# Performance work log

Hardware: AMD Instinct MI355X
Metric: run time of the kernel (lower is better)

The kernel has to match this reference:

```python
import jax, jax.numpy as jnp
import numpy as np

NUM_HEADS = 32
NUM_KV_HEADS = 8
HEAD_DIM = 128
ROPE_THETA = 10000.0


def _rope_cos_sin(seq_len, head_dim, dtype):
    # [seq, head_dim/2] angles, duplicated to [seq, head_dim] via concat (rotate-half convention)
    inv_freq = 1.0 / (ROPE_THETA ** (jnp.arange(0, head_dim, 2, dtype=jnp.float32) / head_dim))
    ang = jnp.arange(seq_len, dtype=jnp.float32)[:, None] * inv_freq[None, :]
    ang = jnp.concatenate([ang, ang], axis=-1)
    return jnp.cos(ang).astype(dtype), jnp.sin(ang).astype(dtype)


def _rotate_half(x):
    d = x.shape[-1] // 2
    return jnp.concatenate([-x[..., d:], x[..., :d]], axis=-1)


def setup_inputs() -> dict:
    key = jax.random.key(0)
    ks = jax.random.split(key, 5)
    E = NUM_HEADS * HEAD_DIM
    KVE = NUM_KV_HEADS * HEAD_DIM
    B, S = 2, 2048
    sc_in = 1.0 / np.sqrt(E)
    return {
        "x": jax.random.normal(ks[0], (B, S, E), jnp.float32),
        "Wq": jax.random.normal(ks[1], (E, E), jnp.float32) * sc_in,
        "Wk": jax.random.normal(ks[2], (E, KVE), jnp.float32) * sc_in,
        "Wv": jax.random.normal(ks[3], (E, KVE), jnp.float32) * sc_in,
        "Wo": jax.random.normal(ks[4], (E, E), jnp.float32) * sc_in,
    }


def reference(x, Wq, Wk, Wv, Wo):
    b, s, e = x.shape
    H, KV, D = NUM_HEADS, NUM_KV_HEADS, HEAD_DIM
    G = H // KV
    scale = 1.0 / np.sqrt(D)

    q = (x @ Wq).reshape(b, s, H, D).transpose(0, 2, 1, 3)    # [b,H,s,D]
    k = (x @ Wk).reshape(b, s, KV, D).transpose(0, 2, 1, 3)   # [b,KV,s,D]
    v = (x @ Wv).reshape(b, s, KV, D).transpose(0, 2, 1, 3)   # [b,KV,s,D]

    cos, sin = _rope_cos_sin(s, D, q.dtype)                   # [s,D]
    q = q * cos + _rotate_half(q) * sin
    k = k * cos + _rotate_half(k) * sin

    # GQA: group q heads by kv head instead of repeat_interleaving k/v
    qg = q.reshape(b, KV, G, s, D)
    attn = jnp.einsum("bkgqd,bkvd->bkgqv", qg, k) * scale     # [b,KV,G,s,s]

    causal = jnp.where(
        jnp.arange(s)[:, None] >= jnp.arange(s)[None, :], 0.0, -jnp.inf
    ).astype(jnp.float32)
    attn = attn.astype(jnp.float32) + causal
    attn = jax.nn.softmax(attn, axis=-1).astype(q.dtype)

    out = jnp.einsum("bkgqv,bkvd->bkgqd", attn, v)            # [b,KV,G,s,D]
    out = out.reshape(b, H, s, D).transpose(0, 2, 1, 3).reshape(b, s, H * D)
    return out @ Wo
```

## Files before the change

### kernel.cpp

```cpp
#include <hip/hip_runtime.h>
#include <stdint.h>
#include <math.h>

typedef short bf16x8 __attribute__((ext_vector_type(8)));
typedef float f32x4 __attribute__((ext_vector_type(4)));

#if __has_builtin(__builtin_amdgcn_exp2f)
#define EXP2F(x) __builtin_amdgcn_exp2f(x)
#else
#define EXP2F(x) exp2f(x)
#endif

static constexpr int Bn   = 2;
static constexpr int Sn   = 2048;
static constexpr int NH   = 32;
static constexpr int NKV  = 8;
static constexpr int Dh   = 128;
static constexpr int En   = NH * Dh;
static constexpr int KVEn = NKV * Dh;
static constexpr int QKVE = En + 2 * KVEn;
static constexpr int MT   = Bn * Sn;
static constexpr int QT   = Sn / 128;

__device__ __forceinline__ unsigned short f2bf(float f) {
  unsigned int u = __float_as_uint(f);
  u += 0x7FFFu + ((u >> 16) & 1u);
  return (unsigned short)(u >> 16);
}
__device__ __forceinline__ float bf2f(unsigned short h) {
  return __uint_as_float(((unsigned int)h) << 16);
}

typedef __attribute__((address_space(1))) void* gas_t;
typedef __attribute__((address_space(3))) void* las_t;
__device__ __forceinline__ void gl_lds16(const void* g, void* l) {
  __builtin_amdgcn_global_load_lds((gas_t)(uintptr_t)g, (las_t)(uint32_t)(uintptr_t)l,
                                   16, 0, 0);
}

#define VMW(n)  asm volatile("s_waitcnt vmcnt(" #n ")" ::: "memory")
#define LGKM0   asm volatile("s_waitcnt lgkmcnt(0)" ::: "memory")
#define SCHEDB  __builtin_amdgcn_sched_barrier(0)
#define BAR     __builtin_amdgcn_s_barrier()


__global__ void cast_bf16_kernel(const float* __restrict__ x,
                                 unsigned short* __restrict__ y, int n4) {
  int i = blockIdx.x * 256 + threadIdx.x;
  if (i >= n4) return;
  float4 v = ((const float4*)x)[i];
  ushort4 o;
  o.x = f2bf(v.x); o.y = f2bf(v.y); o.z = f2bf(v.z); o.w = f2bf(v.w);
  ((ushort4*)y)[i] = o;
}

__global__ void tcast_kernel(const float* __restrict__ W,
                             unsigned short* __restrict__ WT, int R, int C) {
  __shared__ float t[32][33];
  int tx = threadIdx.x, ty = threadIdx.y;
  int c = blockIdx.x * 32 + tx, r = blockIdx.y * 32 + ty;
  t[ty][tx] = W[(size_t)r * C + c];
  __syncthreads();
  int ro = blockIdx.x * 32 + ty, co = blockIdx.y * 32 + tx;
  WT[(size_t)ro * R + co] = f2bf(t[tx][ty]);
}

__global__ void rope_table_kernel(float2* __restrict__ cs) {
  int i = blockIdx.x * 256 + threadIdx.x;
  int s = i >> 6, d = i & 63;
  float inv = powf(10000.0f, -(float)d * (1.0f / 64.0f));
  float a = (float)s * inv;
  cs[i] = make_float2(cosf(a), sinf(a));
}

__global__ void rope_kernel(unsigned short* __restrict__ q,
                            const float2* __restrict__ cs, int rowstride, float scl) {
  int row = blockIdx.x;
  int s = row & (Sn - 1);
  int hl = threadIdx.x >> 6, d = threadIdx.x & 63;
  int h = blockIdx.y * 4 + hl;
  size_t base = (size_t)row * rowstride + (size_t)h * Dh + d;
  float2 c = cs[s * 64 + d];
  float x0 = bf2f(q[base]), x1 = bf2f(q[base + 64]);
  q[base]      = f2bf((x0 * c.x - x1 * c.y) * scl);
  q[base + 64] = f2bf((x1 * c.x + x0 * c.y) * scl);
}

__global__ void vtrans_kernel(const unsigned short* __restrict__ V, int rowstride,
                              unsigned short* __restrict__ Vt) {
  __shared__ unsigned short t[32][33];
  int bk = blockIdx.z;
  int b = bk >> 3, kv = bk & 7;
  int d = blockIdx.x * 32 + threadIdx.x;
  int s = blockIdx.y * 32 + threadIdx.y;
  t[threadIdx.y][threadIdx.x] = V[(size_t)(b * Sn + s) * rowstride + kv * Dh + d];
  __syncthreads();
  int dd = blockIdx.x * 32 + threadIdx.y;
  int so = blockIdx.y * 32 + threadIdx.x;
  Vt[((size_t)bk * Dh + dd) * Sn + so] = t[threadIdx.x][threadIdx.y];
}


__global__ __launch_bounds__(512, 2) void gemm256_kernel(
    const unsigned short* __restrict__ A, const unsigned short* __restrict__ BT,
    void* __restrict__ Cout, int M, int N, int K, int out_f32) {
  __shared__ unsigned short lds[2][4][128 * 64];
  const int tid = threadIdx.x;
  const int lane = tid & 63, wave = tid >> 6;
  const int r15 = lane & 15, kg = lane >> 4;
  const int wr = wave >> 2, wc = wave & 3;
  const int m0 = blockIdx.y * 256, n0 = blockIdx.x * 256;
  const char* Ab = (const char*)A;
  const char* Bb = (const char*)BT;
  const int KT = K >> 6;

  f32x4 acc[2][2][4][2] = {};
  bf16x8 ar[4][2];
  bf16x8 br[2][2][2];

#define STAGE_H(SRC, ROW0, KT_, SLOT)                                         \
  do {                                                                        \
    _Pragma("unroll") for (int ld = 0; ld < 2; ++ld) {                        \
      int _f = (ld * 512 + tid) * 16;                                         \
      int _row = _f >> 7, _cb = _f & 127;                                     \
      gl_lds16(SRC + ((size_t)((ROW0) + _row) * K + (KT_) * 64) * 2 +         \
                   (_cb ^ ((_row & 7) << 4)),                                 \
               (char*)(SLOT) + _f);                                           \
    }                                                                         \
  } while (0)

#define GPHASE(MH, NH, BUF, DO_LDA, DO_LDB, STAGE_STMT, WAIT_STMT)            \
  do {                                                                        \
    if (DO_LDA) {                                                             \
      const char* _as = (const char*)lds[BUF][MH];                            \
      _Pragma("unroll") for (int mf = 0; mf < 4; ++mf) {                      \
        int _r = wr * 64 + mf * 16 + r15;                                     \
        int _sw = (_r & 7) << 4;                                              \
        ar[mf][0] = *(const bf16x8*)(_as + _r * 128 + ((kg * 16) ^ _sw));     \
        ar[mf][1] = *(const bf16x8*)(_as + _r * 128 + ((64 + kg * 16) ^ _sw));\
      }                                                                       \
    }                                                                         \
    if (DO_LDB) {                                                             \
      const char* _bs = (const char*)lds[BUF][2 + NH];                        \
      _Pragma("unroll") for (int nf = 0; nf < 2; ++nf) {                      \
        int _r = wc * 32 + nf * 16 + r15;                                     \
        int _sw = (_r & 7) << 4;                                              \
        br[NH][nf][0] =                                                       \
            *(const bf16x8*)(_bs + _r * 128 + ((kg * 16) ^ _sw));             \
        br[NH][nf][1] =                                                       \
            *(const bf16x8*)(_bs + _r * 128 + ((64 + kg * 16) ^ _sw));        \
      }                                                                       \
    }                                                                         \
    STAGE_STMT;                                                               \
    BAR;                                                                      \
    if ((DO_LDA) || (DO_LDB)) { LGKM0; }                                      \
    SCHEDB;                                                                   \
    __builtin_amdgcn_s_setprio(1);                                            \
    _Pragma("unroll") for (int mf = 0; mf < 4; ++mf)                          \
      _Pragma("unroll") for (int nf = 0; nf < 2; ++nf) {                      \
        acc[MH][NH][mf][nf] = __builtin_amdgcn_mfma_f32_16x16x32_bf16(        \
            ar[mf][0], br[NH][nf][0], acc[MH][NH][mf][nf], 0, 0, 0);          \
        acc[MH][NH][mf][nf] = __builtin_amdgcn_mfma_f32_16x16x32_bf16(        \
            ar[mf][1], br[NH][nf][1], acc[MH][NH][mf][nf], 0, 0, 0);          \
      }                                                                       \
    __builtin_amdgcn_s_setprio(0);                                            \
    SCHEDB;                                                                   \
    WAIT_STMT;                                                                \
    BAR;                                                                      \
    SCHEDB;                                                                   \
  } while (0)

  STAGE_H(Ab, m0,       0, lds[0][0]);
  STAGE_H(Bb, n0,       0, lds[0][2]);
  STAGE_H(Ab, m0 + 128, 0, lds[0][1]);
  STAGE_H(Bb, n0 + 128, 0, lds[0][3]);
  STAGE_H(Ab, m0,       1, lds[1][0]);
  STAGE_H(Bb, n0,       1, lds[1][2]);
  VMW(8);
  SCHEDB;
  BAR;
  SCHEDB;

  for (int k = 0; k + 2 < KT; k += 2) {
    GPHASE(0, 0, 0, true,  true,  STAGE_H(Ab, m0 + 128, k + 1, lds[1][1]), VMW(6));
    GPHASE(0, 1, 0, false, true,  STAGE_H(Bb, n0 + 128, k + 1, lds[1][3]), VMW(10));
    GPHASE(1, 0, 0, true,  false, STAGE_H(Ab, m0,       k + 2, lds[0][0]), (void)0);
    GPHASE(1, 1, 0, false, false, STAGE_H(Bb, n0,       k + 2, lds[0][2]), VMW(8));
    GPHASE(0, 0, 1, true,  true,  STAGE_H(Ab, m0 + 128, k + 2, lds[0][1]), VMW(6));
    GPHASE(0, 1, 1, false, true,  STAGE_H(Bb, n0 + 128, k + 2, lds[0][3]), VMW(10));
    GPHASE(1, 0, 1, true,  false, STAGE_H(Ab, m0,       k + 3, lds[1][0]), (void)0);
    GPHASE(1, 1, 1, false, false, STAGE_H(Bb, n0,       k + 3, lds[1][2]), VMW(8));
  }
  GPHASE(0, 0, 0, true,  true,  STAGE_H(Ab, m0 + 128, KT - 1, lds[1][1]), VMW(6));
  GPHASE(0, 1, 0, false, true,  STAGE_H(Bb, n0 + 128, KT - 1, lds[1][3]), VMW(10));
  GPHASE(1, 0, 0, true,  false, (void)0, (void)0);
  GPHASE(1, 1, 0, false, false, (void)0, VMW(0));
  GPHASE(0, 0, 1, true,  true,  (void)0, (void)0);
  GPHASE(0, 1, 1, false, true,  (void)0, (void)0);
  GPHASE(1, 0, 1, true,  false, (void)0, (void)0);
  GPHASE(1, 1, 1, false, false, (void)0, (void)0);

#undef GPHASE
#undef STAGE_H

#pragma unroll
  for (int mh = 0; mh < 2; ++mh)
#pragma unroll
    for (int nh = 0; nh < 2; ++nh)
#pragma unroll
      for (int mf = 0; mf < 4; ++mf)
#pragma unroll
        for (int nf = 0; nf < 2; ++nf)
#pragma unroll
          for (int t = 0; t < 4; ++t) {
            int row = m0 + mh * 128 + wr * 64 + mf * 16 + kg * 4 + t;
            int col = n0 + nh * 128 + wc * 32 + nf * 16 + r15;
            if (out_f32)
              ((float*)Cout)[(size_t)row * N + col] = acc[mh][nh][mf][nf][t];
            else
              ((unsigned short*)Cout)[(size_t)row * N + col] =
                  f2bf(acc[mh][nh][mf][nf][t]);
          }
}


__device__ __forceinline__ void sm_update(f32x4 sc[4], f32x4 o[8],
                                          float mrow[4], float lrow[4],
                                          bool diag, int qrow0, int kt,
                                          int r15, int kg, char* Pw) {
  if (diag) {
#pragma unroll
    for (int kf = 0; kf < 4; ++kf) {
      int kvg = kt * 64 + kf * 16 + r15;
#pragma unroll
      for (int t = 0; t < 4; ++t)
        if (kvg > qrow0 + kg * 4 + t) sc[kf][t] = -1e30f;
    }
  }
  float mx[4], sm[4];
#pragma unroll
  for (int t = 0; t < 4; ++t) {
    float v = fmaxf(fmaxf(sc[0][t], sc[1][t]), fmaxf(sc[2][t], sc[3][t]));
#pragma unroll
    for (int off = 1; off < 16; off <<= 1) v = fmaxf(v, __shfl_xor(v, off, 16));
    mx[t] = fmaxf(mrow[t], v);
    sm[t] = EXP2F(mrow[t] - mx[t]);
    mrow[t] = mx[t];
  }
#pragma unroll
  for (int kf = 0; kf < 4; ++kf)
#pragma unroll
    for (int t = 0; t < 4; ++t) sc[kf][t] = EXP2F(sc[kf][t] - mx[t]);
#pragma unroll
  for (int t = 0; t < 4; ++t) {
    float v = sc[0][t] + sc[1][t] + sc[2][t] + sc[3][t];
#pragma unroll
    for (int off = 1; off < 16; off <<= 1) v += __shfl_xor(v, off, 16);
    lrow[t] = lrow[t] * sm[t] + v;
  }
#pragma unroll
  for (int nf = 0; nf < 8; ++nf)
#pragma unroll
    for (int t = 0; t < 4; ++t) o[nf][t] *= sm[t];
#pragma unroll
  for (int kf = 0; kf < 4; ++kf)
#pragma unroll
    for (int t = 0; t < 4; ++t) {
      int r = kg * 4 + t, c = kf * 16 + r15;
      *(unsigned short*)(Pw + r * 128 + ((c * 2) ^ ((r & 7) << 4))) = f2bf(sc[kf][t]);
    }
}

__global__ __launch_bounds__(512, 4) void attn_kernel(
    const unsigned short* __restrict__ Q, const unsigned short* __restrict__ Kl,
    const unsigned short* __restrict__ Vt, unsigned short* __restrict__ AO) {
  __shared__ unsigned short Ks[2][64 * 128];
  __shared__ unsigned short Vs[2][128 * 64];
  __shared__ unsigned short Ps[8][16 * 64];
  const int tid = threadIdx.x, lane = tid & 63, wave = tid >> 6;
  const int h = blockIdx.x, b = blockIdx.z;
  const int qt = (QT - 1) - blockIdx.y;
  const int kvh = h >> 2;
  const int r15 = lane & 15, kg = lane >> 4;
  const int qrow0 = qt * 128 + wave * 16;
  const int kmax = 2 * qt + 2;

  bf16x8 qf[4];
#pragma unroll
  for (int db = 0; db < 4; ++db)
    qf[db] = *(const bf16x8*)&Q[(size_t)(b * Sn + qrow0 + r15) * QKVE +
                                h * Dh + db * 32 + kg * 8];

  f32x4 o[8] = {};
  float mrow[4] = {-1e30f, -1e30f, -1e30f, -1e30f};
  float lrow[4] = {0.f, 0.f, 0.f, 0.f};

  const char* Kbase = (const char*)Kl + (size_t)(b * Sn) * (QKVE * 2) + kvh * 256;
  const char* Vbase = (const char*)Vt + (size_t)((b * NKV + kvh) * Dh) * (Sn * 2);

  auto stage = [&](int kt, int bi) {
#pragma unroll
    for (int c = 0; c < 2; ++c) {
      int f = (c * 512 + tid) * 16;
      int row = f >> 8, cb = f & 255;
      gl_lds16(Kbase + (size_t)(kt * 64 + row) * (QKVE * 2) + (cb ^ ((row & 7) << 4)),
               (char*)Ks[bi] + f);
    }
#pragma unroll
    for (int c = 0; c < 2; ++c) {
      int f = (c * 512 + tid) * 16;
      int row = f >> 7, cb = f & 127;
      gl_lds16(Vbase + (size_t)row * (Sn * 2) + kt * 128 + (cb ^ ((row & 7) << 4)),
               (char*)Vs[bi] + f);
    }
  };

  stage(0, 0);
  __syncthreads();

  for (int kt = 0; kt < kmax; ++kt) {
    const int cur = kt & 1;
    if (kt + 1 < kmax) stage(kt + 1, cur ^ 1);
    if (kt * 64 <= qrow0 + 15) {
      const char* Kc = (const char*)Ks[cur];
      const char* Vc = (const char*)Vs[cur];
      f32x4 sc[4] = {};
      __builtin_amdgcn_s_setprio(1);
#pragma unroll
      for (int db = 0; db < 4; ++db) {
#pragma unroll
        for (int kf = 0; kf < 4; ++kf) {
          int krow = kf * 16 + r15;
          int cb = (db * 32 + kg * 8) * 2;
          bf16x8 kb = *(const bf16x8*)(Kc + krow * 256 + (cb ^ ((krow & 7) << 4)));
          sc[kf] = __builtin_amdgcn_mfma_f32_16x16x32_bf16(qf[db], kb, sc[kf], 0, 0, 0);
        }
      }
      __builtin_amdgcn_s_setprio(0);

      char* Pw = (char*)Ps[wave];
      bool diag = (kt * 64 + 63) > qrow0;
      sm_update(sc, o, mrow, lrow, diag, qrow0, kt, r15, kg, Pw);

      __builtin_amdgcn_s_setprio(1);
#pragma unroll
      for (int ks = 0; ks < 2; ++ks) {
        bf16x8 pa = *(const bf16x8*)(Pw + r15 * 128 + ((kg * 16 + ks * 64) ^ ((r15 & 7) << 4)));
#pragma unroll
        for (int nf = 0; nf < 8; ++nf) {
          int vrow = nf * 16 + r15;
          int cb = (ks * 32 + kg * 8) * 2;
          bf16x8 vb = *(const bf16x8*)(Vc + vrow * 128 + (cb ^ ((vrow & 7) << 4)));
          o[nf] = __builtin_amdgcn_mfma_f32_16x16x32_bf16(pa, vb, o[nf], 0, 0, 0);
        }
      }
      __builtin_amdgcn_s_setprio(0);
    }
    __syncthreads();
  }

  float rinv[4];
#pragma unroll
  for (int t = 0; t < 4; ++t) rinv[t] = 1.0f / lrow[t];
#pragma unroll
  for (int nf = 0; nf < 8; ++nf)
#pragma unroll
    for (int t = 0; t < 4; ++t) {
      int srow = qrow0 + kg * 4 + t;
      AO[(size_t)(b * Sn + srow) * En + h * Dh + nf * 16 + r15] = f2bf(o[nf][t] * rinv[t]);
    }
}


extern "C" void kernel_launch(void* const* d_in, const int* in_sizes, int n_in,
                              void* d_out, int out_size, void* d_ws, size_t ws_size,
                              hipStream_t stream) {
  const float* x  = (const float*)d_in[0];
  const float* Wq = (const float*)d_in[1];
  const float* Wk = (const float*)d_in[2];
  const float* Wv = (const float*)d_in[3];
  const float* Wo = (const float*)d_in[4];

  char* ws = (char*)d_ws;
  size_t off = 0;
  auto alloc = [&](size_t bytes) -> char* {
    char* p = ws + off;
    off += (bytes + 255) & ~(size_t)255;
    return p;
  };
  unsigned short* xb   = (unsigned short*)alloc((size_t)MT * En * 2);
  unsigned short* Wqkv = (unsigned short*)alloc((size_t)QKVE * En * 2);
  unsigned short* WoT  = (unsigned short*)alloc((size_t)En * En * 2);
  unsigned short* Cqkv = (unsigned short*)alloc((size_t)MT * QKVE * 2);
  unsigned short* Vt   = (unsigned short*)alloc((size_t)MT * KVEn * 2);
  float2* cs           = (float2*)alloc((size_t)Sn * 64 * sizeof(float2));
  unsigned short* AO   = xb;

  cast_bf16_kernel<<<MT * (En / 4) / 256, 256, 0, stream>>>(x, xb, MT * En / 4);
  tcast_kernel<<<dim3(En / 32, En / 32), dim3(32, 32), 0, stream>>>(Wq, Wqkv, En, En);
  tcast_kernel<<<dim3(KVEn / 32, En / 32), dim3(32, 32), 0, stream>>>(
      Wk, Wqkv + (size_t)En * En, En, KVEn);
  tcast_kernel<<<dim3(KVEn / 32, En / 32), dim3(32, 32), 0, stream>>>(
      Wv, Wqkv + (size_t)(En + KVEn) * En, En, KVEn);
  tcast_kernel<<<dim3(En / 32, En / 32), dim3(32, 32), 0, stream>>>(Wo, WoT, En, En);
  rope_table_kernel<<<Sn * 64 / 256, 256, 0, stream>>>(cs);

  gemm256_kernel<<<dim3(QKVE / 256, MT / 256), 512, 0, stream>>>(
      xb, Wqkv, Cqkv, MT, QKVE, En, 0);

  const float scl = 0.08838834764831845f * 1.4426950408889634f;
  rope_kernel<<<dim3(MT, NH / 4), 256, 0, stream>>>(Cqkv, cs, QKVE, scl);
  rope_kernel<<<dim3(MT, NKV / 4), 256, 0, stream>>>(Cqkv + En, cs, QKVE, 1.0f);
  vtrans_kernel<<<dim3(Dh / 32, Sn / 32, Bn * NKV), dim3(32, 32), 0, stream>>>(
      Cqkv + En + KVEn, QKVE, Vt);

  attn_kernel<<<dim3(NH, QT, Bn), 512, 0, stream>>>(Cqkv, Cqkv + En, Vt, AO);

  gemm256_kernel<<<dim3(En / 256, MT / 256), 512, 0, stream>>>(
      AO, WoT, d_out, MT, En, En, 1);
}
```

Before: 617.9 us.

## Restructure GEMM wave tiling to 128x64 per wave with register double-buffered fragments

```diff
diff --git a/kernel.cpp b/kernel.cpp
--- a/kernel.cpp
+++ b/kernel.cpp
@@ -108,119 +108,126 @@
   const int tid = threadIdx.x;
   const int lane = tid & 63, wave = tid >> 6;
   const int r15 = lane & 15, kg = lane >> 4;
-  const int wr = wave >> 2, wc = wave & 3;
+  const int wm = wave >> 2, wn = wave & 3;
+  const int brow0 = (wn & 1) * 64;
   const int m0 = blockIdx.y * 256, n0 = blockIdx.x * 256;
   const char* Ab = (const char*)A;
   const char* Bb = (const char*)BT;
   const int KT = K >> 6;
 
-  f32x4 acc[2][2][4][2] = {};
-  bf16x8 ar[4][2];
-  bf16x8 br[2][2][2];
-
-#define STAGE_H(SRC, ROW0, KT_, SLOT)                                         \
+  f32x4 acc[8][4] = {};
+  bf16x8 a0[4][2], a1[4][2];
+  bf16x8 bb0[4][2], bb1[4][2];
+
+#define STG(SRC, ROW0, TILE, SLOT)                                            \
   do {                                                                        \
     _Pragma("unroll") for (int ld = 0; ld < 2; ++ld) {                        \
       int _f = (ld * 512 + tid) * 16;                                         \
       int _row = _f >> 7, _cb = _f & 127;                                     \
-      gl_lds16(SRC + ((size_t)((ROW0) + _row) * K + (KT_) * 64) * 2 +         \
+      gl_lds16(SRC + ((size_t)((ROW0) + _row) * K + (size_t)(TILE) * 64) * 2 +\
                    (_cb ^ ((_row & 7) << 4)),                                 \
                (char*)(SLOT) + _f);                                           \
     }                                                                         \
   } while (0)
 
-#define GPHASE(MH, NH, BUF, DO_LDA, DO_LDB, STAGE_STMT, WAIT_STMT)            \
+#define RD_A(DST, BUF, MQ)                                                    \
   do {                                                                        \
-    if (DO_LDA) {                                                             \
-      const char* _as = (const char*)lds[BUF][MH];                            \
-      _Pragma("unroll") for (int mf = 0; mf < 4; ++mf) {                      \
-        int _r = wr * 64 + mf * 16 + r15;                                     \
-        int _sw = (_r & 7) << 4;                                              \
-        ar[mf][0] = *(const bf16x8*)(_as + _r * 128 + ((kg * 16) ^ _sw));     \
-        ar[mf][1] = *(const bf16x8*)(_as + _r * 128 + ((64 + kg * 16) ^ _sw));\
-      }                                                                       \
+    const char* _b = (const char*)lds[BUF][wm];                               \
+    _Pragma("unroll") for (int j = 0; j < 4; ++j) {                           \
+      int _r = (MQ) * 64 + j * 16 + r15;                                      \
+      int _s = (_r & 7) << 4;                                                 \
+      DST[j][0] = *(const bf16x8*)(_b + _r * 128 + ((kg * 16) ^ _s));         \
+      DST[j][1] = *(const bf16x8*)(_b + _r * 128 + ((64 + kg * 16) ^ _s));    \
     }                                                                         \
-    if (DO_LDB) {                                                             \
-      const char* _bs = (const char*)lds[BUF][2 + NH];                        \
-      _Pragma("unroll") for (int nf = 0; nf < 2; ++nf) {                      \
-        int _r = wc * 32 + nf * 16 + r15;                                     \
-        int _sw = (_r & 7) << 4;                                              \
-        br[NH][nf][0] =                                                       \
-            *(const bf16x8*)(_bs + _r * 128 + ((kg * 16) ^ _sw));             \
-        br[NH][nf][1] =                                                       \
-            *(const bf16x8*)(_bs + _r * 128 + ((64 + kg * 16) ^ _sw));        \
-      }                                                                       \
+  } while (0)
+
+#define RD_B(DST, BUF)                                                        \
+  do {                                                                        \
+    const char* _b = (const char*)lds[BUF][2 + (wn >> 1)];                    \
+    _Pragma("unroll") for (int f = 0; f < 4; ++f) {                           \
+      int _r = brow0 + f * 16 + r15;                                          \
+      int _s = (_r & 7) << 4;                                                 \
+      DST[f][0] = *(const bf16x8*)(_b + _r * 128 + ((kg * 16) ^ _s));         \
+      DST[f][1] = *(const bf16x8*)(_b + _r * 128 + ((64 + kg * 16) ^ _s));    \
     }                                                                         \
-    STAGE_STMT;                                                               \
-    BAR;                                                                      \
-    if ((DO_LDA) || (DO_LDB)) { LGKM0; }                                      \
-    SCHEDB;                                                                   \
+  } while (0)
+
+#define PH(MQ, NQ, AB, BB, RD, ST, WT, DOBAR)                                 \
+  do {                                                                        \
+    RD;                                                                       \
+    ST;                                                                       \
     __builtin_amdgcn_s_setprio(1);                                            \
-    _Pragma("unroll") for (int mf = 0; mf < 4; ++mf)                          \
-      _Pragma("unroll") for (int nf = 0; nf < 2; ++nf) {                      \
-        acc[MH][NH][mf][nf] = __builtin_amdgcn_mfma_f32_16x16x32_bf16(        \
-            ar[mf][0], br[NH][nf][0], acc[MH][NH][mf][nf], 0, 0, 0);          \
-        acc[MH][NH][mf][nf] = __builtin_amdgcn_mfma_f32_16x16x32_bf16(        \
-            ar[mf][1], br[NH][nf][1], acc[MH][NH][mf][nf], 0, 0, 0);          \
+    _Pragma("unroll") for (int j = 0; j < 4; ++j)                             \
+      _Pragma("unroll") for (int n2 = 0; n2 < 2; ++n2) {                      \
+        acc[(MQ)*4 + j][(NQ)*2 + n2] =                                        \
+            __builtin_amdgcn_mfma_f32_16x16x32_bf16(                          \
+                AB[j][0], BB[(NQ)*2 + n2][0], acc[(MQ)*4 + j][(NQ)*2 + n2],   \
+                0, 0, 0);                                                     \
+        acc[(MQ)*4 + j][(NQ)*2 + n2] =                                        \
+            __builtin_amdgcn_mfma_f32_16x16x32_bf16(                          \
+                AB[j][1], BB[(NQ)*2 + n2][1], acc[(MQ)*4 + j][(NQ)*2 + n2],   \
+                0, 0, 0);                                                     \
       }                                                                       \
     __builtin_amdgcn_s_setprio(0);                                            \
+    LGKM0;                                                                    \
     SCHEDB;                                                                   \
-    WAIT_STMT;                                                                \
-    BAR;                                                                      \
-    SCHEDB;                                                                   \
+    WT;                                                                       \
+    if (DOBAR) { BAR; SCHEDB; }                                               \
   } while (0)
 
-  STAGE_H(Ab, m0,       0, lds[0][0]);
-  STAGE_H(Bb, n0,       0, lds[0][2]);
-  STAGE_H(Ab, m0 + 128, 0, lds[0][1]);
-  STAGE_H(Bb, n0 + 128, 0, lds[0][3]);
-  STAGE_H(Ab, m0,       1, lds[1][0]);
-  STAGE_H(Bb, n0,       1, lds[1][2]);
-  VMW(8);
+  STG(Bb, n0,       0, lds[0][2]); STG(Bb, n0 + 128, 0, lds[0][3]);
+  STG(Ab, m0,       0, lds[0][0]); STG(Ab, m0 + 128, 0, lds[0][1]);
+  STG(Bb, n0,       1, lds[1][2]); STG(Bb, n0 + 128, 1, lds[1][3]);
+  STG(Ab, m0,       1, lds[1][0]); STG(Ab, m0 + 128, 1, lds[1][1]);
+  VMW(0);
   SCHEDB;
   BAR;
   SCHEDB;
-
-  for (int k = 0; k + 2 < KT; k += 2) {
-    GPHASE(0, 0, 0, true,  true,  STAGE_H(Ab, m0 + 128, k + 1, lds[1][1]), VMW(6));
-    GPHASE(0, 1, 0, false, true,  STAGE_H(Bb, n0 + 128, k + 1, lds[1][3]), VMW(10));
-    GPHASE(1, 0, 0, true,  false, STAGE_H(Ab, m0,       k + 2, lds[0][0]), (void)0);
-    GPHASE(1, 1, 0, false, false, STAGE_H(Bb, n0,       k + 2, lds[0][2]), VMW(8));
-    GPHASE(0, 0, 1, true,  true,  STAGE_H(Ab, m0 + 128, k + 2, lds[0][1]), VMW(6));
-    GPHASE(0, 1, 1, false, true,  STAGE_H(Bb, n0 + 128, k + 2, lds[0][3]), VMW(10));
-    GPHASE(1, 0, 1, true,  false, STAGE_H(Ab, m0,       k + 3, lds[1][0]), (void)0);
-    GPHASE(1, 1, 1, false, false, STAGE_H(Bb, n0,       k + 3, lds[1][2]), VMW(8));
+  RD_B(bb0, 0);
+  RD_A(a0, 0, 0);
+  LGKM0;
+  SCHEDB;
+
+  for (int i = 0; i + 1 < (KT >> 1); ++i) {
+    const int t2 = 2 * i + 2, t3 = 2 * i + 3;
+    PH(0, 0, a0, bb0, RD_A(a1, 0, 1), STG(Bb, n0,       t2, lds[0][2]), VMW(8), 1);
+    PH(0, 1, a0, bb0, (void)0,        STG(Bb, n0 + 128, t2, lds[0][3]), VMW(8), 1);
+    PH(1, 0, a1, bb0, RD_B(bb1, 1),
+       STG(Ab, m0, t2, lds[0][0]); STG(Ab, m0 + 128, t2, lds[0][1]),    VMW(8), 1);
+    PH(1, 1, a1, bb0, RD_A(a0, 1, 0), (void)0,                          VMW(8), 1);
+    PH(0, 0, a0, bb1, RD_A(a1, 1, 1), STG(Bb, n0,       t3, lds[1][2]), VMW(8), 1);
+    PH(0, 1, a0, bb1, (void)0,        STG(Bb, n0 + 128, t3, lds[1][3]), VMW(8), 1);
+    PH(1, 0, a1, bb1, RD_B(bb0, 0),
+       STG(Ab, m0, t3, lds[1][0]); STG(Ab, m0 + 128, t3, lds[1][1]),    VMW(8), 1);
+    PH(1, 1, a1, bb1, RD_A(a0, 0, 0), (void)0,                          VMW(8), 1);
   }
-  GPHASE(0, 0, 0, true,  true,  STAGE_H(Ab, m0 + 128, KT - 1, lds[1][1]), VMW(6));
-  GPHASE(0, 1, 0, false, true,  STAGE_H(Bb, n0 + 128, KT - 1, lds[1][3]), VMW(10));
-  GPHASE(1, 0, 0, true,  false, (void)0, (void)0);
-  GPHASE(1, 1, 0, false, false, (void)0, VMW(0));
-  GPHASE(0, 0, 1, true,  true,  (void)0, (void)0);
-  GPHASE(0, 1, 1, false, true,  (void)0, (void)0);
-  GPHASE(1, 0, 1, true,  false, (void)0, (void)0);
-  GPHASE(1, 1, 1, false, false, (void)0, (void)0);
-
-#undef GPHASE
-#undef STAGE_H
-
-#pragma unroll
-  for (int mh = 0; mh < 2; ++mh)
-#pragma unroll
-    for (int nh = 0; nh < 2; ++nh)
-#pragma unroll
-      for (int mf = 0; mf < 4; ++mf)
-#pragma unroll
-        for (int nf = 0; nf < 2; ++nf)
-#pragma unroll
-          for (int t = 0; t < 4; ++t) {
-            int row = m0 + mh * 128 + wr * 64 + mf * 16 + kg * 4 + t;
-            int col = n0 + nh * 128 + wc * 32 + nf * 16 + r15;
-            if (out_f32)
-              ((float*)Cout)[(size_t)row * N + col] = acc[mh][nh][mf][nf][t];
-            else
-              ((unsigned short*)Cout)[(size_t)row * N + col] =
-                  f2bf(acc[mh][nh][mf][nf][t]);
-          }
+  PH(0, 0, a0, bb0, RD_A(a1, 0, 1), (void)0, VMW(4), 1);
+  PH(0, 1, a0, bb0, (void)0,        (void)0, VMW(0), 1);
+  PH(1, 0, a1, bb0, RD_B(bb1, 1),   (void)0, (void)0, 0);
+  PH(1, 1, a1, bb0, RD_A(a0, 1, 0), (void)0, (void)0, 0);
+  PH(0, 0, a0, bb1, RD_A(a1, 1, 1), (void)0, (void)0, 0);
+  PH(0, 1, a0, bb1, (void)0,        (void)0, (void)0, 0);
+  PH(1, 0, a1, bb1, (void)0,        (void)0, (void)0, 0);
+  PH(1, 1, a1, bb1, (void)0,        (void)0, (void)0, 0);
+
+#undef PH
+#undef RD_B
+#undef RD_A
+#undef STG
+
+#pragma unroll
+  for (int mf = 0; mf < 8; ++mf)
+#pragma unroll
+    for (int nf = 0; nf < 4; ++nf)
+#pragma unroll
+      for (int t = 0; t < 4; ++t) {
+        int row = m0 + wm * 128 + mf * 16 + kg * 4 + t;
+        int col = n0 + wn * 64 + nf * 16 + r15;
+        if (out_f32)
+          ((float*)Cout)[(size_t)row * N + col] = acc[mf][nf][t];
+        else
+          ((unsigned short*)Cout)[(size_t)row * N + col] = f2bf(acc[mf][nf][t]);
+      }
 }
 
 
```

Result: slower. 1.592 ms (+157.6%).

## Software-pipeline LDS fragment reads one phase ahead in GEMM main loop

Applied to the files above, without the earlier changes.

```diff
diff --git a/kernel.cpp b/kernel.cpp
--- a/kernel.cpp
+++ b/kernel.cpp
@@ -115,7 +115,7 @@
   const int KT = K >> 6;
 
   f32x4 acc[2][2][4][2] = {};
-  bf16x8 ar[4][2];
+  bf16x8 aA[4][2], aB[4][2];
   bf16x8 br[2][2][2];
 
 #define STAGE_H(SRC, ROW0, KT_, SLOT)                                         \
@@ -123,49 +123,52 @@
     _Pragma("unroll") for (int ld = 0; ld < 2; ++ld) {                        \
       int _f = (ld * 512 + tid) * 16;                                         \
       int _row = _f >> 7, _cb = _f & 127;                                     \
-      gl_lds16(SRC + ((size_t)((ROW0) + _row) * K + (KT_) * 64) * 2 +         \
+      gl_lds16(SRC + ((size_t)((ROW0) + _row) * K + (size_t)(KT_) * 64) * 2 + \
                    (_cb ^ ((_row & 7) << 4)),                                 \
                (char*)(SLOT) + _f);                                           \
     }                                                                         \
   } while (0)
 
-#define GPHASE(MH, NH, BUF, DO_LDA, DO_LDB, STAGE_STMT, WAIT_STMT)            \
+#define RD_A(DST, BUF, MQ)                                                    \
   do {                                                                        \
-    if (DO_LDA) {                                                             \
-      const char* _as = (const char*)lds[BUF][MH];                            \
-      _Pragma("unroll") for (int mf = 0; mf < 4; ++mf) {                      \
-        int _r = wr * 64 + mf * 16 + r15;                                     \
-        int _sw = (_r & 7) << 4;                                              \
-        ar[mf][0] = *(const bf16x8*)(_as + _r * 128 + ((kg * 16) ^ _sw));     \
-        ar[mf][1] = *(const bf16x8*)(_as + _r * 128 + ((64 + kg * 16) ^ _sw));\
-      }                                                                       \
+    const char* _as = (const char*)lds[BUF][MQ];                              \
+    _Pragma("unroll") for (int mf = 0; mf < 4; ++mf) {                        \
+      int _r = wr * 64 + mf * 16 + r15;                                       \
+      int _sw = (_r & 7) << 4;                                                \
+      DST[mf][0] = *(const bf16x8*)(_as + _r * 128 + ((kg * 16) ^ _sw));      \
+      DST[mf][1] = *(const bf16x8*)(_as + _r * 128 + ((64 + kg * 16) ^ _sw)); \
     }                                                                         \
-    if (DO_LDB) {                                                             \
-      const char* _bs = (const char*)lds[BUF][2 + NH];                        \
-      _Pragma("unroll") for (int nf = 0; nf < 2; ++nf) {                      \
-        int _r = wc * 32 + nf * 16 + r15;                                     \
-        int _sw = (_r & 7) << 4;                                              \
-        br[NH][nf][0] =                                                       \
-            *(const bf16x8*)(_bs + _r * 128 + ((kg * 16) ^ _sw));             \
-        br[NH][nf][1] =                                                       \
-            *(const bf16x8*)(_bs + _r * 128 + ((64 + kg * 16) ^ _sw));        \
-      }                                                                       \
+  } while (0)
+
+#define RD_B(NHI, BUF)                                                        \
+  do {                                                                        \
+    const char* _bs = (const char*)lds[BUF][2 + (NHI)];                       \
+    _Pragma("unroll") for (int nf = 0; nf < 2; ++nf) {                        \
+      int _r = wc * 32 + nf * 16 + r15;                                       \
+      int _sw = (_r & 7) << 4;                                                \
+      br[NHI][nf][0] = *(const bf16x8*)(_bs + _r * 128 + ((kg * 16) ^ _sw));  \
+      br[NHI][nf][1] =                                                        \
+          *(const bf16x8*)(_bs + _r * 128 + ((64 + kg * 16) ^ _sw));          \
     }                                                                         \
+  } while (0)
+
+#define GPHASE(MH, NH, ABANK, STAGE_STMT, WAIT_STMT, TAIL_STMT)               \
+  do {                                                                        \
     STAGE_STMT;                                                               \
-    BAR;                                                                      \
-    if ((DO_LDA) || (DO_LDB)) { LGKM0; }                                      \
+    WAIT_STMT;                                                                \
+    LGKM0;                                                                    \
     SCHEDB;                                                                   \
+    TAIL_STMT;                                                                \
     __builtin_amdgcn_s_setprio(1);                                            \
     _Pragma("unroll") for (int mf = 0; mf < 4; ++mf)                          \
-      _Pragma("unroll") for (int nf = 0; nf < 2; ++nf) {                      \
-        acc[MH][NH][mf][nf] = __builtin_amdgcn_mfma_f32_16x16x32_bf16(        \
-            ar[mf][0], br[NH][nf][0], acc[MH][NH][mf][nf], 0, 0, 0);          \
-        acc[MH][NH][mf][nf] = __builtin_amdgcn_mfma_f32_16x16x32_bf16(        \
-            ar[mf][1], br[NH][nf][1], acc[MH][NH][mf][nf], 0, 0, 0);          \
+      _Pragma("unroll") for (int n2 = 0; n2 < 2; ++n2) {                      \
+        acc[MH][NH][mf][n2] = __builtin_amdgcn_mfma_f32_16x16x32_bf16(        \
+            ABANK[mf][0], br[NH][n2][0], acc[MH][NH][mf][n2], 0, 0, 0);       \
+        acc[MH][NH][mf][n2] = __builtin_amdgcn_mfma_f32_16x16x32_bf16(        \
+            ABANK[mf][1], br[NH][n2][1], acc[MH][NH][mf][n2], 0, 0, 0);       \
       }                                                                       \
     __builtin_amdgcn_s_setprio(0);                                            \
     SCHEDB;                                                                   \
-    WAIT_STMT;                                                                \
     BAR;                                                                      \
     SCHEDB;                                                                   \
   } while (0)
@@ -180,27 +183,34 @@
   SCHEDB;
   BAR;
   SCHEDB;
-
-  for (int k = 0; k + 2 < KT; k += 2) {
-    GPHASE(0, 0, 0, true,  true,  STAGE_H(Ab, m0 + 128, k + 1, lds[1][1]), VMW(6));
-    GPHASE(0, 1, 0, false, true,  STAGE_H(Bb, n0 + 128, k + 1, lds[1][3]), VMW(10));
-    GPHASE(1, 0, 0, true,  false, STAGE_H(Ab, m0,       k + 2, lds[0][0]), (void)0);
-    GPHASE(1, 1, 0, false, false, STAGE_H(Bb, n0,       k + 2, lds[0][2]), VMW(8));
-    GPHASE(0, 0, 1, true,  true,  STAGE_H(Ab, m0 + 128, k + 2, lds[0][1]), VMW(6));
-    GPHASE(0, 1, 1, false, true,  STAGE_H(Bb, n0 + 128, k + 2, lds[0][3]), VMW(10));
-    GPHASE(1, 0, 1, true,  false, STAGE_H(Ab, m0,       k + 3, lds[1][0]), (void)0);
-    GPHASE(1, 1, 1, false, false, STAGE_H(Bb, n0,       k + 3, lds[1][2]), VMW(8));
+  RD_A(aA, 0, 0);
+  RD_B(0, 0);
+
+  for (int i = 0; i + 1 < (KT >> 1); ++i) {
+    const int t2 = 2 * i + 2, t3 = 2 * i + 3;
+    GPHASE(0, 0, aA, STAGE_H(Ab, m0 + 128, t2 - 1, lds[1][1]), VMW(6),  RD_B(1, 0));
+    GPHASE(0, 1, aA, STAGE_H(Bb, n0 + 128, t2 - 1, lds[1][3]), VMW(10), RD_A(aB, 0, 1));
+    GPHASE(1, 0, aB, STAGE_H(Ab, m0,       t2,     lds[0][0]), (void)0, (void)0);
+    GPHASE(1, 1, aB, STAGE_H(Bb, n0,       t2,     lds[0][2]), VMW(8),
+           RD_A(aA, 1, 0); RD_B(0, 1));
+    GPHASE(0, 0, aA, STAGE_H(Ab, m0 + 128, t2,     lds[0][1]), VMW(6),  RD_B(1, 1));
+    GPHASE(0, 1, aA, STAGE_H(Bb, n0 + 128, t2,     lds[0][3]), VMW(10), RD_A(aB, 1, 1));
+    GPHASE(1, 0, aB, STAGE_H(Ab, m0,       t3,     lds[1][0]), (void)0, (void)0);
+    GPHASE(1, 1, aB, STAGE_H(Bb, n0,       t3,     lds[1][2]), VMW(8),
+           RD_A(aA, 0, 0); RD_B(0, 0));
   }
-  GPHASE(0, 0, 0, true,  true,  STAGE_H(Ab, m0 + 128, KT - 1, lds[1][1]), VMW(6));
-  GPHASE(0, 1, 0, false, true,  STAGE_H(Bb, n0 + 128, KT - 1, lds[1][3]), VMW(10));
-  GPHASE(1, 0, 0, true,  false, (void)0, (void)0);
-  GPHASE(1, 1, 0, false, false, (void)0, VMW(0));
-  GPHASE(0, 0, 1, true,  true,  (void)0, (void)0);
-  GPHASE(0, 1, 1, false, true,  (void)0, (void)0);
-  GPHASE(1, 0, 1, true,  false, (void)0, (void)0);
-  GPHASE(1, 1, 1, false, false, (void)0, (void)0);
+  GPHASE(0, 0, aA, STAGE_H(Ab, m0 + 128, KT - 1, lds[1][1]), VMW(6), RD_B(1, 0));
+  GPHASE(0, 1, aA, STAGE_H(Bb, n0 + 128, KT - 1, lds[1][3]), (void)0, RD_A(aB, 0, 1));
+  GPHASE(1, 0, aB, (void)0, (void)0, (void)0);
+  GPHASE(1, 1, aB, (void)0, VMW(4),  RD_A(aA, 1, 0); RD_B(0, 1));
+  GPHASE(0, 0, aA, (void)0, VMW(0),  RD_B(1, 1));
+  GPHASE(0, 1, aA, (void)0, (void)0, RD_A(aB, 1, 1));
+  GPHASE(1, 0, aB, (void)0, (void)0, (void)0);
+  GPHASE(1, 1, aB, (void)0, (void)0, (void)0);
 
 #undef GPHASE
+#undef RD_B
+#undef RD_A
 #undef STAGE_H
 
 #pragma unroll
```

After: 1.273 ms. 2.06x slower.
